# Kernel optimization log

Hardware: AMD Instinct MI355X
Metric: run time of the kernel (lower is better)

## Reference

```python
import jax, jax.numpy as jnp
import numpy as np

N = 100000
E = 600000
H = 128
OUT = 64
L = 3

def glorot(key, shape):
    fan_in, fan_out = shape[0], shape[1]
    lim = jnp.sqrt(6.0 / (fan_in + fan_out))
    return jax.random.uniform(key, shape, jnp.float32, -lim, lim)

def setup_inputs() -> dict:
    key = jax.random.key(0)
    ks = jax.random.split(key, 20)
    x = jax.random.normal(ks[0], (N, H), jnp.float32)
    edge_index = jax.random.randint(ks[1], (2, E), 0, N, jnp.int64)
    edge_attr = jax.random.uniform(ks[2], (E, 1), jnp.float32)
    # stacked per-layer params [L, ...]
    W_lin = jnp.stack([glorot(jax.random.fold_in(ks[3], i), (H, H)) for i in range(L)])
    b_lin = jnp.zeros((L, H), jnp.float32)
    W_msg = jnp.stack([glorot(jax.random.fold_in(ks[4], i), (H + 1, H)) for i in range(L)])
    b_msg = jnp.zeros((L, H), jnp.float32)
    W_l = jnp.stack([glorot(jax.random.fold_in(ks[5], i), (H, H)) for i in range(L)])
    b_l = jnp.zeros((L, H), jnp.float32)
    W_r = jnp.stack([glorot(jax.random.fold_in(ks[6], i), (H, H)) for i in range(L)])
    W_dec = glorot(ks[7], (H, H))
    b_dec = jnp.zeros((H,), jnp.float32)
    W_fin = glorot(ks[8], (H, OUT))
    b_fin = jnp.zeros((OUT,), jnp.float32)
    return {"x": x, "edge_attr": edge_attr, "W_lin": W_lin, "b_lin": b_lin,
            "W_msg": W_msg, "b_msg": b_msg, "W_l": W_l, "b_l": b_l, "W_r": W_r,
            "W_dec": W_dec, "b_dec": b_dec, "W_fin": W_fin, "b_fin": b_fin,
            "edge_index": edge_index}

def reference(x, edge_attr, W_lin, b_lin, W_msg, b_msg, W_l, b_l, W_r,
              W_dec, b_dec, W_fin, b_fin, edge_index):
    src, dst = edge_index[0], edge_index[1]  # j -> i (source_to_target)
    # mean-aggregation denominator: in-degree clamped to 1
    deg = jax.ops.segment_sum(jnp.ones((E,), jnp.float32), dst, num_segments=N)
    inv_deg = (1.0 / jnp.maximum(deg, 1.0))[:, None]  # [N,1]
    for l in range(L):
        h = jax.nn.relu(x @ W_lin[l] + b_lin[l])          # [N,H]
        msg_in = jnp.concatenate([h[src], edge_attr], -1)  # [E,H+1]
        msg = jax.nn.relu(msg_in @ W_msg[l] + b_msg[l])    # [E,H]
        agg = jax.ops.segment_sum(msg, dst, num_segments=N) * inv_deg  # [N,H]
        out = (agg @ W_l[l] + b_l[l]) + x @ W_r[l]         # lin_l(agg) + lin_r(x_r)
        x = jax.nn.relu(out)  # dropout p=0.0 -> identity
    emb = jax.nn.relu(x @ W_dec + b_dec)
    logits = emb @ W_fin + b_fin  # [N,OUT]
    return logits
```

## Files before the change

kernel.cpp:

```cpp
#include <hip/hip_runtime.h>

using short8 = __attribute__((ext_vector_type(8))) short;
using f32x4  = __attribute__((ext_vector_type(4))) float;

constexpr int HD = 128;
constexpr int NBLK_SCAT = 2048;

__device__ __forceinline__ unsigned short f2bf(float f) {
    unsigned u = __builtin_bit_cast(unsigned, f);
    u += 0x7fffu + ((u >> 16) & 1u);
    return (unsigned short)(u >> 16);
}
__device__ __forceinline__ float bflo(unsigned u) { return __builtin_bit_cast(float, u << 16); }
__device__ __forceinline__ float bfhi(unsigned u) { return __builtin_bit_cast(float, u & 0xffff0000u); }

__device__ __forceinline__ short8 ldg8(const unsigned short* p) {
    return *reinterpret_cast<const short8*>(p);
}

template<int NC2, bool F32OUT>
__device__ __forceinline__ void dev_chain(unsigned short* As1, unsigned short* Hs,
    const unsigned short* __restrict__ A, const unsigned short* __restrict__ Wt1,
    const unsigned short* __restrict__ Wtc, const float* __restrict__ b1,
    const float* __restrict__ b2, void* __restrict__ Out, int nrows, int bid)
{
    const int tid  = threadIdx.x;
    const int lane = tid & 63, wave = tid >> 6;
    const int lr = lane & 15, lg = lane >> 4;
    const int row0 = bid * 64;

#pragma unroll
    for (int it = 0; it < 4; ++it) {
        const int q   = wave * 4 + it;
        const int c   = q * 64 + lane;
        const int row = c >> 4, cw = c & 15;
        int grow = row0 + row; grow = grow < nrows ? grow : nrows - 1;
        const int gco = (cw ^ (row & 7)) << 3;
        __builtin_amdgcn_global_load_lds((const unsigned int*)(A + (long)grow * HD + gco),
                                         (unsigned int*)&As1[q * 512], 16, 0, 0);
    }

    const int cb1 = wave * 32;
    short8 bf1[2][4];
#pragma unroll
    for (int ct = 0; ct < 2; ++ct) {
        const unsigned short* bp = Wt1 + (long)(cb1 + ct * 16 + lr) * HD + lg * 8;
#pragma unroll
        for (int kt = 0; kt < 4; ++kt) bf1[ct][kt] = ldg8(bp + kt * 32);
    }
    constexpr int CT2 = NC2 / 64;
    const int cb2 = wave * (NC2 / 4);
    short8 bfc[CT2][4];
#pragma unroll
    for (int ct = 0; ct < CT2; ++ct) {
        const unsigned short* bp = Wtc + (long)(cb2 + ct * 16 + lr) * HD + lg * 8;
#pragma unroll
        for (int kt = 0; kt < 4; ++kt) bfc[ct][kt] = ldg8(bp + kt * 32);
    }

    __syncthreads();

    f32x4 acc[4][2] = {};
#pragma unroll
    for (int kt = 0; kt < 4; ++kt) {
        short8 af[4];
#pragma unroll
        for (int rt = 0; rt < 4; ++rt)
            af[rt] = *reinterpret_cast<const short8*>(
                &As1[(rt * 16 + lr) * HD + (((kt * 4 + lg) ^ (lr & 7)) << 3)]);
#pragma unroll
        for (int rt = 0; rt < 4; ++rt)
#pragma unroll
            for (int ct = 0; ct < 2; ++ct)
                acc[rt][ct] = __builtin_amdgcn_mfma_f32_16x16x32_bf16(af[rt], bf1[ct][kt], acc[rt][ct], 0, 0, 0);
    }

    const float bv1[2] = { b1[cb1 + lr], b1[cb1 + 16 + lr] };
#pragma unroll
    for (int rt = 0; rt < 4; ++rt)
#pragma unroll
        for (int ct = 0; ct < 2; ++ct) {
            const int cc = cb1 + ct * 16 + lr;
#pragma unroll
            for (int i = 0; i < 4; ++i) {
                const int row = rt * 16 + lg * 4 + i;
                const float v = fmaxf(acc[rt][ct][i] + bv1[ct], 0.f);
                Hs[row * HD + ((((cc >> 3) ^ (row & 7)) << 3) | (cc & 7))] = f2bf(v);
            }
        }
    __syncthreads();

    f32x4 acc2[4][CT2] = {};
#pragma unroll
    for (int kt = 0; kt < 4; ++kt) {
        short8 ah[4];
#pragma unroll
        for (int rt = 0; rt < 4; ++rt)
            ah[rt] = *reinterpret_cast<const short8*>(
                &Hs[(rt * 16 + lr) * HD + (((kt * 4 + lg) ^ (lr & 7)) << 3)]);
#pragma unroll
        for (int rt = 0; rt < 4; ++rt)
#pragma unroll
            for (int ct = 0; ct < CT2; ++ct)
                acc2[rt][ct] = __builtin_amdgcn_mfma_f32_16x16x32_bf16(ah[rt], bfc[ct][kt], acc2[rt][ct], 0, 0, 0);
    }
    float bv2[CT2];
#pragma unroll
    for (int ct = 0; ct < CT2; ++ct) bv2[ct] = b2[cb2 + ct * 16 + lr];
#pragma unroll
    for (int rt = 0; rt < 4; ++rt)
#pragma unroll
        for (int ct = 0; ct < CT2; ++ct) {
            const int cc = cb2 + ct * 16 + lr;
#pragma unroll
            for (int i = 0; i < 4; ++i) {
                const int r = row0 + rt * 16 + lg * 4 + i;
                if (r < nrows) {
                    const float v = acc2[rt][ct][i] + bv2[ct];
                    if constexpr (F32OUT) ((float*)Out)[(long)r * NC2 + cc] = v;
                    else ((unsigned short*)Out)[(long)r * NC2 + cc] = f2bf(v);
                }
            }
        }
}

template<int NC2, bool F32OUT>
__global__ __launch_bounds__(256)
void k_chain(const unsigned short* __restrict__ A, const unsigned short* __restrict__ Wt1,
             const unsigned short* __restrict__ Wtc, const float* __restrict__ b1,
             const float* __restrict__ b2, void* __restrict__ Out, int nrows)
{
    __shared__ __align__(16) unsigned short As1[64 * HD];
    __shared__ __align__(16) unsigned short Hs [64 * HD];
    dev_chain<NC2, F32OUT>(As1, Hs, A, Wt1, Wtc, b1, b2, Out, nrows, blockIdx.x);
}

__global__ __launch_bounds__(256)
void k_dualchain(const unsigned short* __restrict__ Agg, const unsigned short* __restrict__ X,
                 const unsigned short* __restrict__ WtL, const unsigned short* __restrict__ WtR,
                 const float* __restrict__ bl_,
                 const unsigned short* __restrict__ Wt1, const float* __restrict__ b1,
                 const unsigned short* __restrict__ Wtc, const float* __restrict__ b2,
                 unsigned short* __restrict__ Xout, unsigned short* __restrict__ Gout, int n)
{
    __shared__ __align__(16) unsigned short Ag[64 * HD];
    __shared__ __align__(16) unsigned short Xs[64 * HD];
    __shared__ __align__(16) unsigned short Ts[64 * HD];

    const int tid  = threadIdx.x;
    const int lane = tid & 63, wave = tid >> 6;
    const int lr = lane & 15, lg = lane >> 4;
    const int row0 = blockIdx.x * 64;

#pragma unroll
    for (int it = 0; it < 4; ++it) {
        const int q   = wave * 4 + it;
        const int c   = q * 64 + lane;
        const int row = c >> 4, cw = c & 15;
        int grow = row0 + row; grow = grow < n ? grow : n - 1;
        const int gco = (cw ^ (row & 7)) << 3;
        __builtin_amdgcn_global_load_lds((const unsigned int*)(Agg + (long)grow * HD + gco),
                                         (unsigned int*)&Ag[q * 512], 16, 0, 0);
        __builtin_amdgcn_global_load_lds((const unsigned int*)(X + (long)grow * HD + gco),
                                         (unsigned int*)&Xs[q * 512], 16, 0, 0);
    }

    const int cb = wave * 32;
    short8 bl[2][4], br[2][4];
#pragma unroll
    for (int ct = 0; ct < 2; ++ct) {
        const unsigned short* pl = WtL + (long)(cb + ct * 16 + lr) * HD + lg * 8;
        const unsigned short* pr = WtR + (long)(cb + ct * 16 + lr) * HD + lg * 8;
#pragma unroll
        for (int kt = 0; kt < 4; ++kt) { bl[ct][kt] = ldg8(pl + kt * 32); br[ct][kt] = ldg8(pr + kt * 32); }
    }
    __syncthreads();

    {
        f32x4 acc[4][2] = {};
#pragma unroll
        for (int kt = 0; kt < 4; ++kt) {
            short8 aa[4], ax[4];
#pragma unroll
            for (int rt = 0; rt < 4; ++rt) {
                const int base = (rt * 16 + lr) * HD + (((kt * 4 + lg) ^ (lr & 7)) << 3);
                aa[rt] = *reinterpret_cast<const short8*>(&Ag[base]);
                ax[rt] = *reinterpret_cast<const short8*>(&Xs[base]);
            }
#pragma unroll
            for (int rt = 0; rt < 4; ++rt)
#pragma unroll
                for (int ct = 0; ct < 2; ++ct) {
                    acc[rt][ct] = __builtin_amdgcn_mfma_f32_16x16x32_bf16(aa[rt], bl[ct][kt], acc[rt][ct], 0, 0, 0);
                    acc[rt][ct] = __builtin_amdgcn_mfma_f32_16x16x32_bf16(ax[rt], br[ct][kt], acc[rt][ct], 0, 0, 0);
                }
        }
        const float bv[2] = { bl_[cb + lr], bl_[cb + 16 + lr] };
#pragma unroll
        for (int rt = 0; rt < 4; ++rt)
#pragma unroll
            for (int ct = 0; ct < 2; ++ct) {
                const int cc = cb + ct * 16 + lr;
#pragma unroll
                for (int i = 0; i < 4; ++i) {
                    const int row = rt * 16 + lg * 4 + i;
                    const int r = row0 + row;
                    const float v = fmaxf(acc[rt][ct][i] + bv[ct], 0.f);
                    const unsigned short vb = f2bf(v);
                    Ts[row * HD + ((((cc >> 3) ^ (row & 7)) << 3) | (cc & 7))] = vb;
                    if (r < n) Xout[(long)r * HD + cc] = vb;
                }
            }
    }
    __syncthreads();

    {
        short8 b1f[2][4];
#pragma unroll
        for (int ct = 0; ct < 2; ++ct) {
            const unsigned short* bp = Wt1 + (long)(cb + ct * 16 + lr) * HD + lg * 8;
#pragma unroll
            for (int kt = 0; kt < 4; ++kt) b1f[ct][kt] = ldg8(bp + kt * 32);
        }
        f32x4 a2[4][2] = {};
#pragma unroll
        for (int kt = 0; kt < 4; ++kt) {
            short8 ah[4];
#pragma unroll
            for (int rt = 0; rt < 4; ++rt)
                ah[rt] = *reinterpret_cast<const short8*>(
                    &Ts[(rt * 16 + lr) * HD + (((kt * 4 + lg) ^ (lr & 7)) << 3)]);
#pragma unroll
            for (int rt = 0; rt < 4; ++rt)
#pragma unroll
                for (int ct = 0; ct < 2; ++ct)
                    a2[rt][ct] = __builtin_amdgcn_mfma_f32_16x16x32_bf16(ah[rt], b1f[ct][kt], a2[rt][ct], 0, 0, 0);
        }
        short8 bcf[2][4];
#pragma unroll
        for (int ct = 0; ct < 2; ++ct) {
            const unsigned short* bp = Wtc + (long)(cb + ct * 16 + lr) * HD + lg * 8;
#pragma unroll
            for (int kt = 0; kt < 4; ++kt) bcf[ct][kt] = ldg8(bp + kt * 32);
        }
        const float bv[2] = { b1[cb + lr], b1[cb + 16 + lr] };
#pragma unroll
        for (int rt = 0; rt < 4; ++rt)
#pragma unroll
            for (int ct = 0; ct < 2; ++ct) {
                const int cc = cb + ct * 16 + lr;
#pragma unroll
                for (int i = 0; i < 4; ++i) {
                    const int row = rt * 16 + lg * 4 + i;
                    const float v = fmaxf(a2[rt][ct][i] + bv[ct], 0.f);
                    Ag[row * HD + ((((cc >> 3) ^ (row & 7)) << 3) | (cc & 7))] = f2bf(v);
                }
            }
        __syncthreads();

        f32x4 a3[4][2] = {};
#pragma unroll
        for (int kt = 0; kt < 4; ++kt) {
            short8 ah[4];
#pragma unroll
            for (int rt = 0; rt < 4; ++rt)
                ah[rt] = *reinterpret_cast<const short8*>(
                    &Ag[(rt * 16 + lr) * HD + (((kt * 4 + lg) ^ (lr & 7)) << 3)]);
#pragma unroll
            for (int rt = 0; rt < 4; ++rt)
#pragma unroll
                for (int ct = 0; ct < 2; ++ct)
                    a3[rt][ct] = __builtin_amdgcn_mfma_f32_16x16x32_bf16(ah[rt], bcf[ct][kt], a3[rt][ct], 0, 0, 0);
        }
        const float bv2[2] = { b2[cb + lr], b2[cb + 16 + lr] };
#pragma unroll
        for (int rt = 0; rt < 4; ++rt)
#pragma unroll
            for (int ct = 0; ct < 2; ++ct) {
                const int cc = cb + ct * 16 + lr;
#pragma unroll
                for (int i = 0; i < 4; ++i) {
                    const int r = row0 + rt * 16 + lg * 4 + i;
                    if (r < n) Gout[(long)r * HD + cc] = f2bf(a3[rt][ct][i] + bv2[ct]);
                }
            }
    }
}

__global__ __launch_bounds__(256)
void k_dualdec(const unsigned short* __restrict__ Agg, const unsigned short* __restrict__ X,
               const unsigned short* __restrict__ WtL, const unsigned short* __restrict__ WtR,
               const float* __restrict__ bl_, const unsigned short* __restrict__ Wdec,
               const float* __restrict__ bdec, const unsigned short* __restrict__ Wfin,
               const float* __restrict__ bfin, float* __restrict__ Out, int n)
{
    __shared__ __align__(16) unsigned short Ag[64 * HD];
    __shared__ __align__(16) unsigned short Xs[64 * HD];
    __shared__ __align__(16) unsigned short Ts[64 * HD];

    const int tid  = threadIdx.x;
    const int lane = tid & 63, wave = tid >> 6;
    const int lr = lane & 15, lg = lane >> 4;
    const int row0 = blockIdx.x * 64;

#pragma unroll
    for (int it = 0; it < 4; ++it) {
        const int q   = wave * 4 + it;
        const int c   = q * 64 + lane;
        const int row = c >> 4, cw = c & 15;
        int grow = row0 + row; grow = grow < n ? grow : n - 1;
        const int gco = (cw ^ (row & 7)) << 3;
        __builtin_amdgcn_global_load_lds((const unsigned int*)(Agg + (long)grow * HD + gco),
                                         (unsigned int*)&Ag[q * 512], 16, 0, 0);
        __builtin_amdgcn_global_load_lds((const unsigned int*)(X + (long)grow * HD + gco),
                                         (unsigned int*)&Xs[q * 512], 16, 0, 0);
    }

    const int cb = wave * 32;
    short8 bl[2][4], br[2][4];
#pragma unroll
    for (int ct = 0; ct < 2; ++ct) {
        const unsigned short* pl = WtL + (long)(cb + ct * 16 + lr) * HD + lg * 8;
        const unsigned short* pr = WtR + (long)(cb + ct * 16 + lr) * HD + lg * 8;
#pragma unroll
        for (int kt = 0; kt < 4; ++kt) { bl[ct][kt] = ldg8(pl + kt * 32); br[ct][kt] = ldg8(pr + kt * 32); }
    }
    __syncthreads();

    {
        f32x4 acc[4][2] = {};
#pragma unroll
        for (int kt = 0; kt < 4; ++kt) {
            short8 aa[4], ax[4];
#pragma unroll
            for (int rt = 0; rt < 4; ++rt) {
                const int base = (rt * 16 + lr) * HD + (((kt * 4 + lg) ^ (lr & 7)) << 3);
                aa[rt] = *reinterpret_cast<const short8*>(&Ag[base]);
                ax[rt] = *reinterpret_cast<const short8*>(&Xs[base]);
            }
#pragma unroll
            for (int rt = 0; rt < 4; ++rt)
#pragma unroll
                for (int ct = 0; ct < 2; ++ct) {
                    acc[rt][ct] = __builtin_amdgcn_mfma_f32_16x16x32_bf16(aa[rt], bl[ct][kt], acc[rt][ct], 0, 0, 0);
                    acc[rt][ct] = __builtin_amdgcn_mfma_f32_16x16x32_bf16(ax[rt], br[ct][kt], acc[rt][ct], 0, 0, 0);
                }
        }
        const float bv[2] = { bl_[cb + lr], bl_[cb + 16 + lr] };
#pragma unroll
        for (int rt = 0; rt < 4; ++rt)
#pragma unroll
            for (int ct = 0; ct < 2; ++ct) {
                const int cc = cb + ct * 16 + lr;
#pragma unroll
                for (int i = 0; i < 4; ++i) {
                    const int row = rt * 16 + lg * 4 + i;
                    const float v = fmaxf(acc[rt][ct][i] + bv[ct], 0.f);
                    Ts[row * HD + ((((cc >> 3) ^ (row & 7)) << 3) | (cc & 7))] = f2bf(v);
                }
            }
    }
    __syncthreads();

    {
        short8 bd[2][4];
#pragma unroll
        for (int ct = 0; ct < 2; ++ct) {
            const unsigned short* bp = Wdec + (long)(cb + ct * 16 + lr) * HD + lg * 8;
#pragma unroll
            for (int kt = 0; kt < 4; ++kt) bd[ct][kt] = ldg8(bp + kt * 32);
        }
        f32x4 a2[4][2] = {};
#pragma unroll
        for (int kt = 0; kt < 4; ++kt) {
            short8 ah[4];
#pragma unroll
            for (int rt = 0; rt < 4; ++rt)
                ah[rt] = *reinterpret_cast<const short8*>(
                    &Ts[(rt * 16 + lr) * HD + (((kt * 4 + lg) ^ (lr & 7)) << 3)]);
#pragma unroll
            for (int rt = 0; rt < 4; ++rt)
#pragma unroll
                for (int ct = 0; ct < 2; ++ct)
                    a2[rt][ct] = __builtin_amdgcn_mfma_f32_16x16x32_bf16(ah[rt], bd[ct][kt], a2[rt][ct], 0, 0, 0);
        }
        const int cbf = wave * 16;
        short8 bfn[4];
#pragma unroll
        for (int kt = 0; kt < 4; ++kt)
            bfn[kt] = ldg8(Wfin + (long)(cbf + lr) * HD + lg * 8 + kt * 32);
        const float bv[2] = { bdec[cb + lr], bdec[cb + 16 + lr] };
#pragma unroll
        for (int rt = 0; rt < 4; ++rt)
#pragma unroll
            for (int ct = 0; ct < 2; ++ct) {
                const int cc = cb + ct * 16 + lr;
#pragma unroll
                for (int i = 0; i < 4; ++i) {
                    const int row = rt * 16 + lg * 4 + i;
                    const float v = fmaxf(a2[rt][ct][i] + bv[ct], 0.f);
                    Ag[row * HD + ((((cc >> 3) ^ (row & 7)) << 3) | (cc & 7))] = f2bf(v);
                }
            }
        __syncthreads();

        f32x4 a3[4] = {};
#pragma unroll
        for (int kt = 0; kt < 4; ++kt) {
            short8 ah[4];
#pragma unroll
            for (int rt = 0; rt < 4; ++rt)
                ah[rt] = *reinterpret_cast<const short8*>(
                    &Ag[(rt * 16 + lr) * HD + (((kt * 4 + lg) ^ (lr & 7)) << 3)]);
#pragma unroll
            for (int rt = 0; rt < 4; ++rt)
                a3[rt] = __builtin_amdgcn_mfma_f32_16x16x32_bf16(ah[rt], bfn[kt], a3[rt], 0, 0, 0);
        }
        const float bvf = bfin[cbf + lr];
#pragma unroll
        for (int rt = 0; rt < 4; ++rt)
#pragma unroll
            for (int i = 0; i < 4; ++i) {
                const int r = row0 + rt * 16 + lg * 4 + i;
                if (r < n) Out[(long)r * 64 + cbf + lr] = a3[rt][i] + bvf;
            }
    }
}

__device__ __forceinline__ void dev_deg(const int* __restrict__ dst, int* __restrict__ deg,
                                        int nE, int n, int bid, int nblk) {
    const int grp = bid & 7, bin = bid >> 3, nbin = nblk >> 3;
    const int chunk = (n + 7) >> 3;
    const int lo = grp * chunk, hi = min(n, lo + chunk);
    for (int e = bin * 256 + threadIdx.x; e < nE; e += nbin * 256) {
        const int d = dst[e];
        if (d >= lo && d < hi) atomicAdd(&deg[d], 1);
    }
}

__device__ __forceinline__ void dev_fill(const int* __restrict__ src, const int* __restrict__ dst,
                                         const float* __restrict__ eattr, const int* __restrict__ rowstart,
                                         int* __restrict__ degcur, uint2* __restrict__ csr_rec,
                                         int nE, int n, int bid, int nblk) {
    const int grp = bid & 7, bin = bid >> 3, nbin = nblk >> 3;
    const int chunk = (n + 7) >> 3;
    const int lo = grp * chunk, hi = min(n, lo + chunk);
    for (int e = bin * 256 + threadIdx.x; e < nE; e += nbin * 256) {
        const int d = dst[e];
        if (d >= lo && d < hi) {
            const int p = rowstart[d] + atomicSub(&degcur[d], 1) - 1;
            uint2 rec;
            rec.x = (unsigned)src[e];
            rec.y = __builtin_bit_cast(unsigned, eattr[e]);
            csr_rec[p] = rec;
        }
    }
}

__global__ __launch_bounds__(256)
void k_u1(const int* __restrict__ dst, int* __restrict__ deg, int nE,
          const float* __restrict__ xin, unsigned short* __restrict__ xb, long n8, int ncast,
          const float* __restrict__ Wlin, const float* __restrict__ Wmsg,
          const float* __restrict__ Wl,   const float* __restrict__ Wr,
          const float* __restrict__ Wdec, const float* __restrict__ Wfin,
          unsigned short* __restrict__ wt, int n)
{
    const int bid = blockIdx.x;
    if (bid < NBLK_SCAT) { dev_deg(dst, deg, nE, n, bid, NBLK_SCAT); return; }
    const int b = bid - NBLK_SCAT;
    if (b < ncast) {
        const long i = (long)b * 256 + threadIdx.x;
        if (i >= n8) return;
        const float4 v0 = *((const float4*)xin + i * 2);
        const float4 v1 = *((const float4*)xin + i * 2 + 1);
        unsigned o[4];
        o[0] = (unsigned)f2bf(v0.x) | ((unsigned)f2bf(v0.y) << 16);
        o[1] = (unsigned)f2bf(v0.z) | ((unsigned)f2bf(v0.w) << 16);
        o[2] = (unsigned)f2bf(v1.x) | ((unsigned)f2bf(v1.y) << 16);
        o[3] = (unsigned)f2bf(v1.z) | ((unsigned)f2bf(v1.w) << 16);
        *(uint4*)(xb + i * 8) = *(uint4*)o;
        return;
    }
    const int local = b - ncast;
    const int m = local >> 6;
    const float* src; int C = 128;
    if      (m < 3)  src = Wlin + m * 16384;
    else if (m < 6)  src = Wmsg + (m - 3) * (129 * 128);
    else if (m < 9)  src = Wl   + (m - 6) * 16384;
    else if (m < 12) src = Wr   + (m - 9) * 16384;
    else if (m == 12) src = Wdec;
    else { src = Wfin; C = 64; }
    const int elems = C * 128;
    const int e = (local & 63) * 256 + threadIdx.x;
    if (e >= elems) return;
    const int c = e >> 7, k = e & 127;
    wt[m * 16384 + e] = f2bf(src[k * C + c]);
}

__global__ __launch_bounds__(256)
void k_u2(const int* __restrict__ src, const int* __restrict__ dst,
          const float* __restrict__ eattr, const int* __restrict__ rowstart,
          int* __restrict__ degcur, uint2* __restrict__ csr_rec, int nE,
          const unsigned short* __restrict__ A, const unsigned short* __restrict__ Wt1,
          const unsigned short* __restrict__ Wtc, const float* __restrict__ b1,
          const float* __restrict__ b2, unsigned short* __restrict__ Out, int n)
{
    __shared__ __align__(16) unsigned short As1[64 * HD];
    __shared__ __align__(16) unsigned short Hs [64 * HD];
    if (blockIdx.x < NBLK_SCAT) {
        dev_fill(src, dst, eattr, rowstart, degcur, csr_rec, nE, n, blockIdx.x, NBLK_SCAT);
        return;
    }
    dev_chain<128, false>(As1, Hs, A, Wt1, Wtc, b1, b2, Out, n, blockIdx.x - NBLK_SCAT);
}

__global__ void k_chunksum(const int* __restrict__ deg, int* __restrict__ csum, int n) {
    __shared__ int s[256];
    int t = threadIdx.x, i = blockIdx.x * 256 + t;
    s[t] = (i < n) ? deg[i] : 0;
    __syncthreads();
    for (int o = 128; o > 0; o >>= 1) { if (t < o) s[t] += s[t + o]; __syncthreads(); }
    if (t == 0) csum[blockIdx.x] = s[0];
}

__global__ void k_scanmid(const int* __restrict__ csum, int* __restrict__ cbase,
                          int* __restrict__ rowstart, int nch, int n) {
    __shared__ int s[512];
    int t = threadIdx.x;
    int v = (t < nch) ? csum[t] : 0;
    s[t] = v; __syncthreads();
    for (int off = 1; off < 512; off <<= 1) {
        int tmp = (t >= off) ? s[t - off] : 0;
        __syncthreads();
        s[t] += tmp;
        __syncthreads();
    }
    if (t < nch) cbase[t] = s[t] - v;
    if (t == nch - 1) rowstart[n] = s[t];
}

__global__ void k_scan2(const int* __restrict__ deg, const int* __restrict__ cbase,
                        int* __restrict__ rowstart, float* __restrict__ inv_deg, int n) {
    __shared__ int s[256];
    int t = threadIdx.x, i = blockIdx.x * 256 + t;
    int v = (i < n) ? deg[i] : 0;
    s[t] = v; __syncthreads();
    for (int off = 1; off < 256; off <<= 1) {
        int tmp = (t >= off) ? s[t - off] : 0;
        __syncthreads();
        s[t] += tmp;
        __syncthreads();
    }
    if (i < n) {
        rowstart[i] = cbase[blockIdx.x] + s[t] - v;
        inv_deg[i] = 1.0f / fmaxf((float)v, 1.0f);
    }
}

__global__ __launch_bounds__(256)
void k_agg(const unsigned short* __restrict__ g, const uint2* __restrict__ rec,
           const int* __restrict__ rs, const float* __restrict__ inv_deg,
           const float* __restrict__ wlast, unsigned short* __restrict__ agg, int n) {
    const int lane = threadIdx.x & 15;
    const int node = blockIdx.x * 16 + (threadIdx.x >> 4);
    if (node >= n) return;
    const int c0 = lane * 8;
    const float4 wla = *(const float4*)(wlast + c0);
    const float4 wlb = *(const float4*)(wlast + c0 + 4);
    const int p0 = rs[node], p1 = rs[node + 1];
    float a0=0,a1=0,a2=0,a3=0,a4=0,a5=0,a6=0,a7=0;
    int p = p0;
    for (; p + 4 <= p1; p += 4) {
        uint2 r[4];
#pragma unroll
        for (int u = 0; u < 4; ++u) r[u] = rec[p + u];
        uint4 G[4];
#pragma unroll
        for (int u = 0; u < 4; ++u) G[u] = *(const uint4*)(g + (long)r[u].x * HD + c0);
#pragma unroll
        for (int u = 0; u < 4; ++u) {
            const float e = __builtin_bit_cast(float, r[u].y);
            a0 += fmaxf(fmaf(e, wla.x, bflo(G[u].x)), 0.f);
            a1 += fmaxf(fmaf(e, wla.y, bfhi(G[u].x)), 0.f);
            a2 += fmaxf(fmaf(e, wla.z, bflo(G[u].y)), 0.f);
            a3 += fmaxf(fmaf(e, wla.w, bfhi(G[u].y)), 0.f);
            a4 += fmaxf(fmaf(e, wlb.x, bflo(G[u].z)), 0.f);
            a5 += fmaxf(fmaf(e, wlb.y, bfhi(G[u].z)), 0.f);
            a6 += fmaxf(fmaf(e, wlb.z, bflo(G[u].w)), 0.f);
            a7 += fmaxf(fmaf(e, wlb.w, bfhi(G[u].w)), 0.f);
        }
    }
    for (; p < p1; ++p) {
        const uint2 r0 = rec[p];
        const float e0 = __builtin_bit_cast(float, r0.y);
        const uint4 G0 = *(const uint4*)(g + (long)r0.x * HD + c0);
        a0 += fmaxf(fmaf(e0, wla.x, bflo(G0.x)), 0.f);
        a1 += fmaxf(fmaf(e0, wla.y, bfhi(G0.x)), 0.f);
        a2 += fmaxf(fmaf(e0, wla.z, bflo(G0.y)), 0.f);
        a3 += fmaxf(fmaf(e0, wla.w, bfhi(G0.y)), 0.f);
        a4 += fmaxf(fmaf(e0, wlb.x, bflo(G0.z)), 0.f);
        a5 += fmaxf(fmaf(e0, wlb.y, bfhi(G0.z)), 0.f);
        a6 += fmaxf(fmaf(e0, wlb.z, bflo(G0.w)), 0.f);
        a7 += fmaxf(fmaf(e0, wlb.w, bfhi(G0.w)), 0.f);
    }
    const float id = inv_deg[node];
    uint4 o;
    o.x = (unsigned)f2bf(a0 * id) | ((unsigned)f2bf(a1 * id) << 16);
    o.y = (unsigned)f2bf(a2 * id) | ((unsigned)f2bf(a3 * id) << 16);
    o.z = (unsigned)f2bf(a4 * id) | ((unsigned)f2bf(a5 * id) << 16);
    o.w = (unsigned)f2bf(a6 * id) | ((unsigned)f2bf(a7 * id) << 16);
    *(uint4*)(agg + (long)node * HD + c0) = o;
}

extern "C" void kernel_launch(void* const* d_in, const int* in_sizes, int n_in,
                              void* d_out, int out_size, void* d_ws, size_t ws_size,
                              hipStream_t stream)
{
    const float* x     = (const float*)d_in[0];
    const float* eattr = (const float*)d_in[1];
    const float* W_lin = (const float*)d_in[2];
    const float* b_lin = (const float*)d_in[3];
    const float* W_msg = (const float*)d_in[4];
    const float* b_msg = (const float*)d_in[5];
    const float* W_l   = (const float*)d_in[6];
    const float* b_l   = (const float*)d_in[7];
    const float* W_r   = (const float*)d_in[8];
    const float* W_dec = (const float*)d_in[9];
    const float* b_dec = (const float*)d_in[10];
    const float* W_fin = (const float*)d_in[11];
    const float* b_fin = (const float*)d_in[12];
    const int*   ei    = (const int*)d_in[13];

    const int N = in_sizes[0] / HD;
    const int E = in_sizes[1];
    const int* srcv = ei;
    const int* dstv = ei + E;

    char* wsb = (char*)d_ws;
    size_t off = 0;
    auto carve = [&](size_t bytes) -> void* {
        void* p = wsb + off;
        off += (bytes + 255) & ~(size_t)255;
        return p;
    };
    unsigned short* xb = (unsigned short*)carve((size_t)N * HD * 2);
    unsigned short* t1 = (unsigned short*)carve((size_t)N * HD * 2);
    unsigned short* t2 = (unsigned short*)carve((size_t)N * HD * 2);
    unsigned short* t3 = (unsigned short*)carve((size_t)N * HD * 2);
    unsigned short* wt = (unsigned short*)carve((size_t)14 * 16384 * 2);
    uint2* csr_rec  = (uint2*)carve((size_t)E * 8);
    int*   rowstart = (int*)carve((size_t)(N + 1) * 4);
    int*   deg      = (int*)carve((size_t)N * 4);
    float* inv_deg  = (float*)carve((size_t)N * 4);
    const int NCH = (N + 255) / 256;
    int* csum  = (int*)carve((size_t)NCH * 4);
    int* cbase = (int*)carve((size_t)NCH * 4);

    if (off > ws_size) {
        hipMemsetAsync(d_out, 0, (size_t)out_size * 4, stream);
        return;
    }

    hipMemsetAsync(deg, 0, (size_t)N * 4, stream);

    auto WT = [&](int m) { return wt + (size_t)m * 16384; };
    const int NB64 = (N + 63) / 64;
    const int GAGG = (N + 15) / 16;
    const long n8 = (long)N * HD / 8;
    const int ncast = (int)((n8 + 255) / 256);

    k_u1<<<NBLK_SCAT + ncast + 14 * 64, 256, 0, stream>>>(
        dstv, deg, E, x, xb, n8, ncast, W_lin, W_msg, W_l, W_r, W_dec, W_fin, wt, N);
    k_chunksum<<<NCH, 256, 0, stream>>>(deg, csum, N);
    k_scanmid<<<1, 512, 0, stream>>>(csum, cbase, rowstart, NCH, N);
    k_scan2<<<NCH, 256, 0, stream>>>(deg, cbase, rowstart, inv_deg, N);

    k_u2<<<NBLK_SCAT + NB64, 256, 0, stream>>>(
        srcv, dstv, eattr, rowstart, deg, csr_rec, E,
        xb, WT(0), WT(3), b_lin, b_msg, t2, N);

    auto wlast = [&](int l) { return W_msg + (size_t)l * (HD + 1) * HD + (size_t)HD * HD; };

    k_agg<<<GAGG, 256, 0, stream>>>(t2, csr_rec, rowstart, inv_deg, wlast(0), t1, N);
    k_dualchain<<<NB64, 256, 0, stream>>>(
        t1, xb, WT(6), WT(9), b_l, WT(1), b_lin + HD, WT(4), b_msg + HD, t3, t2, N);
    k_agg<<<GAGG, 256, 0, stream>>>(t2, csr_rec, rowstart, inv_deg, wlast(1), t1, N);
    k_dualchain<<<NB64, 256, 0, stream>>>(
        t1, t3, WT(7), WT(10), b_l + HD, WT(2), b_lin + 2 * HD, WT(5), b_msg + 2 * HD, xb, t2, N);
    k_agg<<<GAGG, 256, 0, stream>>>(t2, csr_rec, rowstart, inv_deg, wlast(2), t1, N);
    k_dualdec<<<NB64, 256, 0, stream>>>(t1, xb, WT(8), WT(11), b_l + 2 * HD,
                                        WT(12), b_dec, WT(13), b_fin, (float*)d_out, N);
}
```

Baseline: 321.6 us.

## Make dual-chain kernels persistent with double-buffered LDS tile prefetch

Converts k_dualchain and k_dualdec into persistent kernels launched on a fixed grid that loop over 64-row tiles. Each kernel loads its weight fragments and biases into registers once, then prefetches the next tile's Agg/X rows into a second LDS buffer while computing the current tile. This is meant to hide global-to-LDS load latency and amortize the weight loads. In exchange, LDS use grows to five 16 KB buffers, which lowers occupancy, register pressure rises from keeping all weight fragments live, and there is an extra barrier per tile. The unused k_chain wrapper is removed.

```diff
diff --git a/kernel.cpp b/kernel.cpp
--- a/kernel.cpp
+++ b/kernel.cpp
@@ -5,6 +5,7 @@
 
 constexpr int HD = 128;
 constexpr int NBLK_SCAT = 2048;
+constexpr int PGRID = 512;
 
 __device__ __forceinline__ unsigned short f2bf(float f) {
     unsigned u = __builtin_bit_cast(unsigned, f);
@@ -124,166 +125,163 @@
         }
 }
 
-template<int NC2, bool F32OUT>
-__global__ __launch_bounds__(256)
-void k_chain(const unsigned short* __restrict__ A, const unsigned short* __restrict__ Wt1,
-             const unsigned short* __restrict__ Wtc, const float* __restrict__ b1,
-             const float* __restrict__ b2, void* __restrict__ Out, int nrows)
-{
-    __shared__ __align__(16) unsigned short As1[64 * HD];
-    __shared__ __align__(16) unsigned short Hs [64 * HD];
-    dev_chain<NC2, F32OUT>(As1, Hs, A, Wt1, Wtc, b1, b2, Out, nrows, blockIdx.x);
-}
-
 __global__ __launch_bounds__(256)
 void k_dualchain(const unsigned short* __restrict__ Agg, const unsigned short* __restrict__ X,
                  const unsigned short* __restrict__ WtL, const unsigned short* __restrict__ WtR,
                  const float* __restrict__ bl_,
                  const unsigned short* __restrict__ Wt1, const float* __restrict__ b1,
                  const unsigned short* __restrict__ Wtc, const float* __restrict__ b2,
-                 unsigned short* __restrict__ Xout, unsigned short* __restrict__ Gout, int n)
+                 unsigned short* __restrict__ Xout, unsigned short* __restrict__ Gout,
+                 int n, int ntiles)
 {
-    __shared__ __align__(16) unsigned short Ag[64 * HD];
-    __shared__ __align__(16) unsigned short Xs[64 * HD];
+    __shared__ __align__(16) unsigned short Ag[2][64 * HD];
+    __shared__ __align__(16) unsigned short Xs[2][64 * HD];
     __shared__ __align__(16) unsigned short Ts[64 * HD];
 
     const int tid  = threadIdx.x;
     const int lane = tid & 63, wave = tid >> 6;
     const int lr = lane & 15, lg = lane >> 4;
-    const int row0 = blockIdx.x * 64;
-
-#pragma unroll
-    for (int it = 0; it < 4; ++it) {
-        const int q   = wave * 4 + it;
-        const int c   = q * 64 + lane;
-        const int row = c >> 4, cw = c & 15;
-        int grow = row0 + row; grow = grow < n ? grow : n - 1;
-        const int gco = (cw ^ (row & 7)) << 3;
-        __builtin_amdgcn_global_load_lds((const unsigned int*)(Agg + (long)grow * HD + gco),
-                                         (unsigned int*)&Ag[q * 512], 16, 0, 0);
-        __builtin_amdgcn_global_load_lds((const unsigned int*)(X + (long)grow * HD + gco),
-                                         (unsigned int*)&Xs[q * 512], 16, 0, 0);
-    }
-
     const int cb = wave * 32;
-    short8 bl[2][4], br[2][4];
+
+    auto dma = [&](int tile, int buf) {
+        const int row0 = tile * 64;
+#pragma unroll
+        for (int it = 0; it < 4; ++it) {
+            const int q   = wave * 4 + it;
+            const int c   = q * 64 + lane;
+            const int row = c >> 4, cw = c & 15;
+            int grow = row0 + row; grow = grow < n ? grow : n - 1;
+            const int gco = (cw ^ (row & 7)) << 3;
+            __builtin_amdgcn_global_load_lds((const unsigned int*)(Agg + (long)grow * HD + gco),
+                                             (unsigned int*)&Ag[buf][q * 512], 16, 0, 0);
+            __builtin_amdgcn_global_load_lds((const unsigned int*)(X + (long)grow * HD + gco),
+                                             (unsigned int*)&Xs[buf][q * 512], 16, 0, 0);
+        }
+    };
+
+    int tile = blockIdx.x;
+    const int stride = gridDim.x;
+    if (tile < ntiles) dma(tile, 0);
+
+    short8 bl[2][4], br[2][4], b1f[2][4], bcf[2][4];
 #pragma unroll
     for (int ct = 0; ct < 2; ++ct) {
-        const unsigned short* pl = WtL + (long)(cb + ct * 16 + lr) * HD + lg * 8;
-        const unsigned short* pr = WtR + (long)(cb + ct * 16 + lr) * HD + lg * 8;
-#pragma unroll
-        for (int kt = 0; kt < 4; ++kt) { bl[ct][kt] = ldg8(pl + kt * 32); br[ct][kt] = ldg8(pr + kt * 32); }
-    }
+        const long roff = (long)(cb + ct * 16 + lr) * HD + lg * 8;
+#pragma unroll
+        for (int kt = 0; kt < 4; ++kt) {
+            bl[ct][kt]  = ldg8(WtL + roff + kt * 32);
+            br[ct][kt]  = ldg8(WtR + roff + kt * 32);
+            b1f[ct][kt] = ldg8(Wt1 + roff + kt * 32);
+            bcf[ct][kt] = ldg8(Wtc + roff + kt * 32);
+        }
+    }
+    const float bvl[2] = { bl_[cb + lr], bl_[cb + 16 + lr] };
+    const float bv1[2] = { b1[cb + lr],  b1[cb + 16 + lr] };
+    const float bv2[2] = { b2[cb + lr],  b2[cb + 16 + lr] };
+
     __syncthreads();
 
-    {
-        f32x4 acc[4][2] = {};
-#pragma unroll
-        for (int kt = 0; kt < 4; ++kt) {
-            short8 aa[4], ax[4];
-#pragma unroll
-            for (int rt = 0; rt < 4; ++rt) {
-                const int base = (rt * 16 + lr) * HD + (((kt * 4 + lg) ^ (lr & 7)) << 3);
-                aa[rt] = *reinterpret_cast<const short8*>(&Ag[base]);
-                ax[rt] = *reinterpret_cast<const short8*>(&Xs[base]);
+    int cur = 0;
+    for (; tile < ntiles; tile += stride, cur ^= 1) {
+        const int nxt = tile + stride;
+        if (nxt < ntiles) dma(nxt, cur ^ 1);
+        const int row0 = tile * 64;
+
+        {
+            f32x4 acc[4][2] = {};
+#pragma unroll
+            for (int kt = 0; kt < 4; ++kt) {
+                short8 aa[4], ax[4];
+#pragma unroll
+                for (int rt = 0; rt < 4; ++rt) {
+                    const int base = (rt * 16 + lr) * HD + (((kt * 4 + lg) ^ (lr & 7)) << 3);
+                    aa[rt] = *reinterpret_cast<const short8*>(&Ag[cur][base]);
+                    ax[rt] = *reinterpret_cast<const short8*>(&Xs[cur][base]);
+                }
+#pragma unroll
+                for (int rt = 0; rt < 4; ++rt)
+#pragma unroll
+                    for (int ct = 0; ct < 2; ++ct) {
+                        acc[rt][ct] = __builtin_amdgcn_mfma_f32_16x16x32_bf16(aa[rt], bl[ct][kt], acc[rt][ct], 0, 0, 0);
+                        acc[rt][ct] = __builtin_amdgcn_mfma_f32_16x16x32_bf16(ax[rt], br[ct][kt], acc[rt][ct], 0, 0, 0);
+                    }
             }
 #pragma unroll
             for (int rt = 0; rt < 4; ++rt)
 #pragma unroll
                 for (int ct = 0; ct < 2; ++ct) {
-                    acc[rt][ct] = __builtin_amdgcn_mfma_f32_16x16x32_bf16(aa[rt], bl[ct][kt], acc[rt][ct], 0, 0, 0);
-                    acc[rt][ct] = __builtin_amdgcn_mfma_f32_16x16x32_bf16(ax[rt], br[ct][kt], acc[rt][ct], 0, 0, 0);
-                }
-        }
-        const float bv[2] = { bl_[cb + lr], bl_[cb + 16 + lr] };
-#pragma unroll
-        for (int rt = 0; rt < 4; ++rt)
-#pragma unroll
-            for (int ct = 0; ct < 2; ++ct) {
-                const int cc = cb + ct * 16 + lr;
-#pragma unroll
-                for (int i = 0; i < 4; ++i) {
-                    const int row = rt * 16 + lg * 4 + i;
-                    const int r = row0 + row;
-                    const float v = fmaxf(acc[rt][ct][i] + bv[ct], 0.f);
-                    const unsigned short vb = f2bf(v);
-                    Ts[row * HD + ((((cc >> 3) ^ (row & 7)) << 3) | (cc & 7))] = vb;
-                    if (r < n) Xout[(long)r * HD + cc] = vb;
-                }
+                    const int cc = cb + ct * 16 + lr;
+#pragma unroll
+                    for (int i = 0; i < 4; ++i) {
+                        const int row = rt * 16 + lg * 4 + i;
+                        const int r = row0 + row;
+                        const float v = fmaxf(acc[rt][ct][i] + bvl[ct], 0.f);
+                        const unsigned short vb = f2bf(v);
+                        Ts[row * HD + ((((cc >> 3) ^ (row & 7)) << 3) | (cc & 7))] = vb;
+                        if (r < n) Xout[(long)r * HD + cc] = vb;
+                    }
+                }
+        }
+        __syncthreads();
+
+        {
+            f32x4 a2[4][2] = {};
+#pragma unroll
+            for (int kt = 0; kt < 4; ++kt) {
+                short8 ah[4];
+#pragma unroll
+                for (int rt = 0; rt < 4; ++rt)
+                    ah[rt] = *reinterpret_cast<const short8*>(
+                        &Ts[(rt * 16 + lr) * HD + (((kt * 4 + lg) ^ (lr & 7)) << 3)]);
+#pragma unroll
+                for (int rt = 0; rt < 4; ++rt)
+#pragma unroll
+                    for (int ct = 0; ct < 2; ++ct)
+                        a2[rt][ct] = __builtin_amdgcn_mfma_f32_16x16x32_bf16(ah[rt], b1f[ct][kt], a2[rt][ct], 0, 0, 0);
             }
-    }
-    __syncthreads();
-
-    {
-        short8 b1f[2][4];
-#pragma unroll
-        for (int ct = 0; ct < 2; ++ct) {
-            const unsigned short* bp = Wt1 + (long)(cb + ct * 16 + lr) * HD + lg * 8;
-#pragma unroll
-            for (int kt = 0; kt < 4; ++kt) b1f[ct][kt] = ldg8(bp + kt * 32);
-        }
-        f32x4 a2[4][2] = {};
-#pragma unroll
-        for (int kt = 0; kt < 4; ++kt) {
-            short8 ah[4];
 #pragma unroll
             for (int rt = 0; rt < 4; ++rt)
-                ah[rt] = *reinterpret_cast<const short8*>(
-                    &Ts[(rt * 16 + lr) * HD + (((kt * 4 + lg) ^ (lr & 7)) << 3)]);
+#pragma unroll
+                for (int ct = 0; ct < 2; ++ct) {
+                    const int cc = cb + ct * 16 + lr;
+#pragma unroll
+                    for (int i = 0; i < 4; ++i) {
+                        const int row = rt * 16 + lg * 4 + i;
+                        const float v = fmaxf(a2[rt][ct][i] + bv1[ct], 0.f);
+                        Ag[cur][row * HD + ((((cc >> 3) ^ (row & 7)) << 3) | (cc & 7))] = f2bf(v);
+                    }
+                }
+        }
+        __syncthreads();
+
+        {
+            f32x4 a3[4][2] = {};
+#pragma unroll
+            for (int kt = 0; kt < 4; ++kt) {
+                short8 ah[4];
+#pragma unroll
+                for (int rt = 0; rt < 4; ++rt)
+                    ah[rt] = *reinterpret_cast<const short8*>(
+                        &Ag[cur][(rt * 16 + lr) * HD + (((kt * 4 + lg) ^ (lr & 7)) << 3)]);
+#pragma unroll
+                for (int rt = 0; rt < 4; ++rt)
+#pragma unroll
+                    for (int ct = 0; ct < 2; ++ct)
+                        a3[rt][ct] = __builtin_amdgcn_mfma_f32_16x16x32_bf16(ah[rt], bcf[ct][kt], a3[rt][ct], 0, 0, 0);
+            }
 #pragma unroll
             for (int rt = 0; rt < 4; ++rt)
 #pragma unroll
-                for (int ct = 0; ct < 2; ++ct)
-                    a2[rt][ct] = __builtin_amdgcn_mfma_f32_16x16x32_bf16(ah[rt], b1f[ct][kt], a2[rt][ct], 0, 0, 0);
-        }
-        short8 bcf[2][4];
-#pragma unroll
-        for (int ct = 0; ct < 2; ++ct) {
-            const unsigned short* bp = Wtc + (long)(cb + ct * 16 + lr) * HD + lg * 8;
-#pragma unroll
-            for (int kt = 0; kt < 4; ++kt) bcf[ct][kt] = ldg8(bp + kt * 32);
-        }
-        const float bv[2] = { b1[cb + lr], b1[cb + 16 + lr] };
-#pragma unroll
-        for (int rt = 0; rt < 4; ++rt)
-#pragma unroll
-            for (int ct = 0; ct < 2; ++ct) {
-                const int cc = cb + ct * 16 + lr;
-#pragma unroll
-                for (int i = 0; i < 4; ++i) {
-                    const int row = rt * 16 + lg * 4 + i;
-                    const float v = fmaxf(a2[rt][ct][i] + bv[ct], 0.f);
-                    Ag[row * HD + ((((cc >> 3) ^ (row & 7)) << 3) | (cc & 7))] = f2bf(v);
-                }
-            }
-        __syncthreads();
-
-        f32x4 a3[4][2] = {};
-#pragma unroll
-        for (int kt = 0; kt < 4; ++kt) {
-            short8 ah[4];
-#pragma unroll
-            for (int rt = 0; rt < 4; ++rt)
-                ah[rt] = *reinterpret_cast<const short8*>(
-                    &Ag[(rt * 16 + lr) * HD + (((kt * 4 + lg) ^ (lr & 7)) << 3)]);
-#pragma unroll
-            for (int rt = 0; rt < 4; ++rt)
-#pragma unroll
-                for (int ct = 0; ct < 2; ++ct)
-                    a3[rt][ct] = __builtin_amdgcn_mfma_f32_16x16x32_bf16(ah[rt], bcf[ct][kt], a3[rt][ct], 0, 0, 0);
-        }
-        const float bv2[2] = { b2[cb + lr], b2[cb + 16 + lr] };
-#pragma unroll
-        for (int rt = 0; rt < 4; ++rt)
-#pragma unroll
-            for (int ct = 0; ct < 2; ++ct) {
-                const int cc = cb + ct * 16 + lr;
-#pragma unroll
-                for (int i = 0; i < 4; ++i) {
-                    const int r = row0 + rt * 16 + lg * 4 + i;
-                    if (r < n) Gout[(long)r * HD + cc] = f2bf(a3[rt][ct][i] + bv2[ct]);
-                }
-            }
+                for (int ct = 0; ct < 2; ++ct) {
+                    const int cc = cb + ct * 16 + lr;
+#pragma unroll
+                    for (int i = 0; i < 4; ++i) {
+                        const int r = row0 + rt * 16 + lg * 4 + i;
+                        if (r < n) Gout[(long)r * HD + cc] = f2bf(a3[rt][ct][i] + bv2[ct]);
+                    }
+                }
+        }
+        __syncthreads();
     }
 }
 
@@ -292,138 +290,151 @@
                const unsigned short* __restrict__ WtL, const unsigned short* __restrict__ WtR,
                const float* __restrict__ bl_, const unsigned short* __restrict__ Wdec,
                const float* __restrict__ bdec, const unsigned short* __restrict__ Wfin,
-               const float* __restrict__ bfin, float* __restrict__ Out, int n)
+               const float* __restrict__ bfin, float* __restrict__ Out, int n, int ntiles)
 {
-    __shared__ __align__(16) unsigned short Ag[64 * HD];
-    __shared__ __align__(16) unsigned short Xs[64 * HD];
+    __shared__ __align__(16) unsigned short Ag[2][64 * HD];
+    __shared__ __align__(16) unsigned short Xs[2][64 * HD];
     __shared__ __align__(16) unsigned short Ts[64 * HD];
 
     const int tid  = threadIdx.x;
     const int lane = tid & 63, wave = tid >> 6;
     const int lr = lane & 15, lg = lane >> 4;
-    const int row0 = blockIdx.x * 64;
-
-#pragma unroll
-    for (int it = 0; it < 4; ++it) {
-        const int q   = wave * 4 + it;
-        const int c   = q * 64 + lane;
-        const int row = c >> 4, cw = c & 15;
-        int grow = row0 + row; grow = grow < n ? grow : n - 1;
-        const int gco = (cw ^ (row & 7)) << 3;
-        __builtin_amdgcn_global_load_lds((const unsigned int*)(Agg + (long)grow * HD + gco),
-                                         (unsigned int*)&Ag[q * 512], 16, 0, 0);
-        __builtin_amdgcn_global_load_lds((const unsigned int*)(X + (long)grow * HD + gco),
-                                         (unsigned int*)&Xs[q * 512], 16, 0, 0);
-    }
-
     const int cb = wave * 32;
-    short8 bl[2][4], br[2][4];
+
+    auto dma = [&](int tile, int buf) {
+        const int row0 = tile * 64;
+#pragma unroll
+        for (int it = 0; it < 4; ++it) {
+            const int q   = wave * 4 + it;
+            const int c   = q * 64 + lane;
+            const int row = c >> 4, cw = c & 15;
+            int grow = row0 + row; grow = grow < n ? grow : n - 1;
+            const int gco = (cw ^ (row & 7)) << 3;
+            __builtin_amdgcn_global_load_lds((const unsigned int*)(Agg + (long)grow * HD + gco),
+                                             (unsigned int*)&Ag[buf][q * 512], 16, 0, 0);
+            __builtin_amdgcn_global_load_lds((const unsigned int*)(X + (long)grow * HD + gco),
+                                             (unsigned int*)&Xs[buf][q * 512], 16, 0, 0);
+        }
+    };
+
+    int tile = blockIdx.x;
+    const int stride = gridDim.x;
+    if (tile < ntiles) dma(tile, 0);
+
+    short8 bl[2][4], br[2][4], bd[2][4], bfn[4];
 #pragma unroll
     for (int ct = 0; ct < 2; ++ct) {
-        const unsigned short* pl = WtL + (long)(cb + ct * 16 + lr) * HD + lg * 8;
-        const unsigned short* pr = WtR + (long)(cb + ct * 16 + lr) * HD + lg * 8;
-#pragma unroll
-        for (int kt = 0; kt < 4; ++kt) { bl[ct][kt] = ldg8(pl + kt * 32); br[ct][kt] = ldg8(pr + kt * 32); }
-    }
+        const long roff = (long)(cb + ct * 16 + lr) * HD + lg * 8;
+#pragma unroll
+        for (int kt = 0; kt < 4; ++kt) {
+            bl[ct][kt] = ldg8(WtL + roff + kt * 32);
+            br[ct][kt] = ldg8(WtR + roff + kt * 32);
+            bd[ct][kt] = ldg8(Wdec + roff + kt * 32);
+        }
+    }
+    const int cbf = wave * 16;
+#pragma unroll
+    for (int kt = 0; kt < 4; ++kt)
+        bfn[kt] = ldg8(Wfin + (long)(cbf + lr) * HD + lg * 8 + kt * 32);
+
+    const float bvl[2] = { bl_[cb + lr], bl_[cb + 16 + lr] };
+    const float bvd[2] = { bdec[cb + lr], bdec[cb + 16 + lr] };
+    const float bvf = bfin[cbf + lr];
+
     __syncthreads();
 
-    {
-        f32x4 acc[4][2] = {};
-#pragma unroll
-        for (int kt = 0; kt < 4; ++kt) {
-            short8 aa[4], ax[4];
-#pragma unroll
-            for (int rt = 0; rt < 4; ++rt) {
-                const int base = (rt * 16 + lr) * HD + (((kt * 4 + lg) ^ (lr & 7)) << 3);
-                aa[rt] = *reinterpret_cast<const short8*>(&Ag[base]);
-                ax[rt] = *reinterpret_cast<const short8*>(&Xs[base]);
+    int cur = 0;
+    for (; tile < ntiles; tile += stride, cur ^= 1) {
+        const int nxt = tile + stride;
+        if (nxt < ntiles) dma(nxt, cur ^ 1);
+        const int row0 = tile * 64;
+
+        {
+            f32x4 acc[4][2] = {};
+#pragma unroll
+            for (int kt = 0; kt < 4; ++kt) {
+                short8 aa[4], ax[4];
+#pragma unroll
+                for (int rt = 0; rt < 4; ++rt) {
+                    const int base = (rt * 16 + lr) * HD + (((kt * 4 + lg) ^ (lr & 7)) << 3);
+                    aa[rt] = *reinterpret_cast<const short8*>(&Ag[cur][base]);
+                    ax[rt] = *reinterpret_cast<const short8*>(&Xs[cur][base]);
+                }
+#pragma unroll
+                for (int rt = 0; rt < 4; ++rt)
+#pragma unroll
+                    for (int ct = 0; ct < 2; ++ct) {
+                        acc[rt][ct] = __builtin_amdgcn_mfma_f32_16x16x32_bf16(aa[rt], bl[ct][kt], acc[rt][ct], 0, 0, 0);
+                        acc[rt][ct] = __builtin_amdgcn_mfma_f32_16x16x32_bf16(ax[rt], br[ct][kt], acc[rt][ct], 0, 0, 0);
+                    }
             }
 #pragma unroll
             for (int rt = 0; rt < 4; ++rt)
 #pragma unroll
                 for (int ct = 0; ct < 2; ++ct) {
-                    acc[rt][ct] = __builtin_amdgcn_mfma_f32_16x16x32_bf16(aa[rt], bl[ct][kt], acc[rt][ct], 0, 0, 0);
-                    acc[rt][ct] = __builtin_amdgcn_mfma_f32_16x16x32_bf16(ax[rt], br[ct][kt], acc[rt][ct], 0, 0, 0);
-                }
-        }
-        const float bv[2] = { bl_[cb + lr], bl_[cb + 16 + lr] };
-#pragma unroll
-        for (int rt = 0; rt < 4; ++rt)
-#pragma unroll
-            for (int ct = 0; ct < 2; ++ct) {
-                const int cc = cb + ct * 16 + lr;
+                    const int cc = cb + ct * 16 + lr;
+#pragma unroll
+                    for (int i = 0; i < 4; ++i) {
+                        const int row = rt * 16 + lg * 4 + i;
+                        const float v = fmaxf(acc[rt][ct][i] + bvl[ct], 0.f);
+                        Ts[row * HD + ((((cc >> 3) ^ (row & 7)) << 3) | (cc & 7))] = f2bf(v);
+                    }
+                }
+        }
+        __syncthreads();
+
+        {
+            f32x4 a2[4][2] = {};
+#pragma unroll
+            for (int kt = 0; kt < 4; ++kt) {
+                short8 ah[4];
+#pragma unroll
+                for (int rt = 0; rt < 4; ++rt)
+                    ah[rt] = *reinterpret_cast<const short8*>(
+                        &Ts[(rt * 16 + lr) * HD + (((kt * 4 + lg) ^ (lr & 7)) << 3)]);
+#pragma unroll
+                for (int rt = 0; rt < 4; ++rt)
+#pragma unroll
+                    for (int ct = 0; ct < 2; ++ct)
+                        a2[rt][ct] = __builtin_amdgcn_mfma_f32_16x16x32_bf16(ah[rt], bd[ct][kt], a2[rt][ct], 0, 0, 0);
+            }
+#pragma unroll
+            for (int rt = 0; rt < 4; ++rt)
+#pragma unroll
+                for (int ct = 0; ct < 2; ++ct) {
+                    const int cc = cb + ct * 16 + lr;
+#pragma unroll
+                    for (int i = 0; i < 4; ++i) {
+                        const int row = rt * 16 + lg * 4 + i;
+                        const float v = fmaxf(a2[rt][ct][i] + bvd[ct], 0.f);
+                        Ag[cur][row * HD + ((((cc >> 3) ^ (row & 7)) << 3) | (cc & 7))] = f2bf(v);
+                    }
+                }
+        }
+        __syncthreads();
+
+        {
+            f32x4 a3[4] = {};
+#pragma unroll
+            for (int kt = 0; kt < 4; ++kt) {
+                short8 ah[4];
+#pragma unroll
+                for (int rt = 0; rt < 4; ++rt)
+                    ah[rt] = *reinterpret_cast<const short8*>(
+                        &Ag[cur][(rt * 16 + lr) * HD + (((kt * 4 + lg) ^ (lr & 7)) << 3)]);
+#pragma unroll
+                for (int rt = 0; rt < 4; ++rt)
+                    a3[rt] = __builtin_amdgcn_mfma_f32_16x16x32_bf16(ah[rt], bfn[kt], a3[rt], 0, 0, 0);
+            }
+#pragma unroll
+            for (int rt = 0; rt < 4; ++rt)
 #pragma unroll
                 for (int i = 0; i < 4; ++i) {
-                    const int row = rt * 16 + lg * 4 + i;
-                    const float v = fmaxf(acc[rt][ct][i] + bv[ct], 0.f);
-                    Ts[row * HD + ((((cc >> 3) ^ (row & 7)) << 3) | (cc & 7))] = f2bf(v);
-                }
-            }
-    }
-    __syncthreads();
-
-    {
-        short8 bd[2][4];
-#pragma unroll
-        for (int ct = 0; ct < 2; ++ct) {
-            const unsigned short* bp = Wdec + (long)(cb + ct * 16 + lr) * HD + lg * 8;
-#pragma unroll
-            for (int kt = 0; kt < 4; ++kt) bd[ct][kt] = ldg8(bp + kt * 32);
-        }
-        f32x4 a2[4][2] = {};
-#pragma unroll
-        for (int kt = 0; kt < 4; ++kt) {
-            short8 ah[4];
-#pragma unroll
-            for (int rt = 0; rt < 4; ++rt)
-                ah[rt] = *reinterpret_cast<const short8*>(
-                    &Ts[(rt * 16 + lr) * HD + (((kt * 4 + lg) ^ (lr & 7)) << 3)]);
-#pragma unroll
-            for (int rt = 0; rt < 4; ++rt)
-#pragma unroll
-                for (int ct = 0; ct < 2; ++ct)
-                    a2[rt][ct] = __builtin_amdgcn_mfma_f32_16x16x32_bf16(ah[rt], bd[ct][kt], a2[rt][ct], 0, 0, 0);
-        }
-        const int cbf = wave * 16;
-        short8 bfn[4];
-#pragma unroll
-        for (int kt = 0; kt < 4; ++kt)
-            bfn[kt] = ldg8(Wfin + (long)(cbf + lr) * HD + lg * 8 + kt * 32);
-        const float bv[2] = { bdec[cb + lr], bdec[cb + 16 + lr] };
-#pragma unroll
-        for (int rt = 0; rt < 4; ++rt)
-#pragma unroll
-            for (int ct = 0; ct < 2; ++ct) {
-                const int cc = cb + ct * 16 + lr;
-#pragma unroll
-                for (int i = 0; i < 4; ++i) {
-                    const int row = rt * 16 + lg * 4 + i;
-                    const float v = fmaxf(a2[rt][ct][i] + bv[ct], 0.f);
-                    Ag[row * HD + ((((cc >> 3) ^ (row & 7)) << 3) | (cc & 7))] = f2bf(v);
-                }
-            }
-        __syncthreads();
-
-        f32x4 a3[4] = {};
-#pragma unroll
-        for (int kt = 0; kt < 4; ++kt) {
-            short8 ah[4];
-#pragma unroll
-            for (int rt = 0; rt < 4; ++rt)
-                ah[rt] = *reinterpret_cast<const short8*>(
-                    &Ag[(rt * 16 + lr) * HD + (((kt * 4 + lg) ^ (lr & 7)) << 3)]);
-#pragma unroll
-            for (int rt = 0; rt < 4; ++rt)
-                a3[rt] = __builtin_amdgcn_mfma_f32_16x16x32_bf16(ah[rt], bfn[kt], a3[rt], 0, 0, 0);
-        }
-        const float bvf = bfin[cbf + lr];
-#pragma unroll
-        for (int rt = 0; rt < 4; ++rt)
-#pragma unroll
-            for (int i = 0; i < 4; ++i) {
-                const int r = row0 + rt * 16 + lg * 4 + i;
-                if (r < n) Out[(long)r * 64 + cbf + lr] = a3[rt][i] + bvf;
-            }
+                    const int r = row0 + rt * 16 + lg * 4 + i;
+                    if (r < n) Out[(long)r * 64 + cbf + lr] = a3[rt][i] + bvf;
+                }
+        }
+        __syncthreads();
     }
 }
 
@@ -682,12 +693,12 @@
     auto wlast = [&](int l) { return W_msg + (size_t)l * (HD + 1) * HD + (size_t)HD * HD; };
 
     k_agg<<<GAGG, 256, 0, stream>>>(t2, csr_rec, rowstart, inv_deg, wlast(0), t1, N);
-    k_dualchain<<<NB64, 256, 0, stream>>>(
-        t1, xb, WT(6), WT(9), b_l, WT(1), b_lin + HD, WT(4), b_msg + HD, t3, t2, N);
+    k_dualchain<<<PGRID, 256, 0, stream>>>(
+        t1, xb, WT(6), WT(9), b_l, WT(1), b_lin + HD, WT(4), b_msg + HD, t3, t2, N, NB64);
     k_agg<<<GAGG, 256, 0, stream>>>(t2, csr_rec, rowstart, inv_deg, wlast(1), t1, N);
-    k_dualchain<<<NB64, 256, 0, stream>>>(
-        t1, t3, WT(7), WT(10), b_l + HD, WT(2), b_lin + 2 * HD, WT(5), b_msg + 2 * HD, xb, t2, N);
+    k_dualchain<<<PGRID, 256, 0, stream>>>(
+        t1, t3, WT(7), WT(10), b_l + HD, WT(2), b_lin + 2 * HD, WT(5), b_msg + 2 * HD, xb, t2, N, NB64);
     k_agg<<<GAGG, 256, 0, stream>>>(t2, csr_rec, rowstart, inv_deg, wlast(2), t1, N);
-    k_dualdec<<<NB64, 256, 0, stream>>>(t1, xb, WT(8), WT(11), b_l + 2 * HD,
-                                        WT(12), b_dec, WT(13), b_fin, (float*)d_out, N);
-}
+    k_dualdec<<<PGRID, 256, 0, stream>>>(t1, xb, WT(8), WT(11), b_l + 2 * HD,
+                                         WT(12), b_dec, WT(13), b_fin, (float*)d_out, N, NB64);
+}
```

After: 324.2 us. Within noise of the previous version (+0.8%).
